# Optimization experiments

Measured on AMD Instinct MI355X. Metric: run time of the kernel, lower is better.

The kernel has to match this reference:

```python
import jax, jax.numpy as jnp
import numpy as np

N_HEADS = 16
MAX_LEN = 4096
D_MODEL = 1024
EPS = 1e-6


def setup_inputs() -> dict:
    key = jax.random.key(0)
    ks = jax.random.split(key, 12)
    B, L, D = 4, 4096, D_MODEL
    s = 1.0 / np.sqrt(D)
    inp = {
        "q": jax.random.normal(ks[0], (B, L, D), jnp.float32),
        "k": jax.random.normal(ks[1], (B, L, D), jnp.float32),
        "v": jax.random.normal(ks[2], (B, L, D), jnp.float32),
        "Wq": jax.random.normal(ks[3], (D, D), jnp.float32) * s,
        "bq": jax.random.normal(ks[4], (D,), jnp.float32) * s,
        "Wk": jax.random.normal(ks[5], (D, D), jnp.float32) * s,
        "bk": jax.random.normal(ks[6], (D,), jnp.float32) * s,
        "Wv": jax.random.normal(ks[7], (D, D), jnp.float32) * s,
        "bv": jax.random.normal(ks[8], (D,), jnp.float32) * s,
        "Wo": jax.random.normal(ks[9], (D, D), jnp.float32) * s,
        "bo": jax.random.normal(ks[10], (D,), jnp.float32) * s,
    }
    return inp


def _cos_attn(q, k, v, Wq, bq, Wk, bk, Wv, bv, Wo, bo):
    B, Lq, D = q.shape
    Lk = k.shape[1]
    H = N_HEADS
    hd = D // H
    # torch Linear: x @ W^T + b
    qh = (q @ Wq.T + bq).reshape(B, Lq, H, hd).transpose(0, 2, 1, 3)  # b h l d
    kh = (k @ Wk.T + bk).reshape(B, Lk, H, hd).transpose(0, 2, 1, 3)
    vh = (v @ Wv.T + bv).reshape(B, Lk, H, hd).transpose(0, 2, 1, 3)
    qh = jax.nn.relu(qh)
    kh = jax.nn.relu(kh)
    # weight_index buffer: pi*(1..max_len)/(2*max_len), shape (1,1,L,1)
    idx = (np.pi * jnp.arange(1, MAX_LEN + 1, dtype=jnp.float32) / (2 * MAX_LEN))
    qi = idx[:Lq][None, None, :, None]
    ki = idx[:Lk][None, None, :, None]
    q_ = jnp.concatenate([qh * jnp.sin(qi), qh * jnp.cos(qi)], axis=-1)  # b h l 2d
    k_ = jnp.concatenate([kh * jnp.sin(ki), kh * jnp.cos(ki)], axis=-1)
    kv_ = jnp.einsum("bnld,bnlm->bndm", k_, vh)  # b h 2d d
    z_ = 1.0 / jnp.maximum(jnp.einsum("bnld,bnd->bnl", q_, jnp.sum(k_, axis=2)), EPS)
    attn = jnp.einsum("bnld,bndm,bnl->bnlm", q_, kv_, z_)  # b h l d
    attn = attn.transpose(0, 2, 1, 3).reshape(B, Lq, D)
    return attn @ Wo.T + bo  # dropout: eval mode (identity)


def reference(q, k, v, Wq, bq, Wk, bk, Wv, bv, Wo, bo):
    return _cos_attn(q, k, v, Wq, bq, Wk, bk, Wv, bv, Wo, bo)
```

## Files before the change

kernel.cpp:

```cpp
#include <hip/hip_runtime.h>

typedef __bf16 bf16x8 __attribute__((ext_vector_type(8)));
typedef float f32x4 __attribute__((ext_vector_type(4)));

#define PI_F 3.14159265358979323846f

__device__ __forceinline__ unsigned short f2bf(float f) {
  unsigned u = __builtin_bit_cast(unsigned, f);
  u += 0x7fffu + ((u >> 16) & 1u);
  return (unsigned short)(u >> 16);
}

__device__ __forceinline__ unsigned scale_pair(unsigned w, float f) {
  const float lo = __builtin_bit_cast(float, w << 16);
  const float hi = __builtin_bit_cast(float, w & 0xffff0000u);
  return (unsigned)f2bf(lo * f) | ((unsigned)f2bf(hi * f) << 16);
}

#define GLD16(gp, lp)                                          \
  __builtin_amdgcn_global_load_lds(                            \
      (const __attribute__((address_space(1))) void*)(gp),     \
      (__attribute__((address_space(3))) void*)(lp), 16, 0, 0)

struct AReg { float4 a0, a1, a2, a3, a4, a5, a6, a7; };

__device__ __forceinline__ uint4 cvtpk16(float4 x, float4 y) {
  unsigned c0, c1, c2, c3;
  asm("v_cvt_pk_bf16_f32 %0, %1, %2" : "=v"(c0) : "v"(x.x), "v"(x.y));
  asm("v_cvt_pk_bf16_f32 %0, %1, %2" : "=v"(c1) : "v"(x.z), "v"(x.w));
  asm("v_cvt_pk_bf16_f32 %0, %1, %2" : "=v"(c2) : "v"(y.x), "v"(y.y));
  asm("v_cvt_pk_bf16_f32 %0, %1, %2" : "=v"(c3) : "v"(y.z), "v"(y.w));
  uint4 u; u.x = c0; u.y = c1; u.z = c2; u.w = c3;
  return u;
}

__device__ __forceinline__ uint2 cvtpk8(float a, float b, float c, float d) {
  unsigned lo, hi;
  asm("v_cvt_pk_bf16_f32 %0, %1, %2" : "=v"(lo) : "v"(a), "v"(b));
  asm("v_cvt_pk_bf16_f32 %0, %1, %2" : "=v"(hi) : "v"(c), "v"(d));
  uint2 r; r.x = lo; r.y = hi;
  return r;
}

__device__ __forceinline__ void unpack8(uint4 w, float* f) {
  f[0] = __builtin_bit_cast(float, w.x << 16);
  f[1] = __builtin_bit_cast(float, w.x & 0xffff0000u);
  f[2] = __builtin_bit_cast(float, w.y << 16);
  f[3] = __builtin_bit_cast(float, w.y & 0xffff0000u);
  f[4] = __builtin_bit_cast(float, w.z << 16);
  f[5] = __builtin_bit_cast(float, w.z & 0xffff0000u);
  f[6] = __builtin_bit_cast(float, w.w << 16);
  f[7] = __builtin_bit_cast(float, w.w & 0xffff0000u);
}

__global__ __launch_bounds__(256) void convert_w(
    const float* __restrict__ Wq, const float* __restrict__ Wk,
    const float* __restrict__ Wv, const float* __restrict__ Wo,
    unsigned short* __restrict__ Wqb, unsigned short* __restrict__ Wkb,
    unsigned short* __restrict__ Wvb, unsigned short* __restrict__ Wob) {
  const int region = blockIdx.y;
  const float* s; unsigned short* d;
  switch (region) {
    case 0: s = Wq; d = Wqb; break;
    case 1: s = Wk; d = Wkb; break;
    case 2: s = Wv; d = Wvb; break;
    default: s = Wo; d = Wob; break;
  }
  const float4* s4 = (const float4*)s;
  ushort4* d4 = (ushort4*)d;
  const int n4 = 262144;
  for (int i = blockIdx.x * 256 + threadIdx.x; i < n4; i += gridDim.x * 256) {
    float4 f = s4[i];
    ushort4 o;
    o.x = f2bf(f.x); o.y = f2bf(f.y); o.z = f2bf(f.z); o.w = f2bf(f.w);
    d4[i] = o;
  }
}

template <int MODE, bool AF32>
__global__ __launch_bounds__(512, 2) void gemm256(
    const void* __restrict__ Ain, const unsigned short* __restrict__ Bw,
    const float* __restrict__ bias, void* __restrict__ out) {
  constexpr int K = 1024, NKT = 16;
  __shared__ unsigned short S[65536];
  const int tid = threadIdx.x;
  const int wave = tid >> 6, lane = tid & 63;
  const int fr = lane & 15, fq = lane >> 4;
  const int wr = wave >> 2, wc = wave & 3;
  const int cpx = gridDim.x >> 3;
  const int wg = (blockIdx.x & 7) * cpx + (blockIdx.x >> 3);
  const int mt = wg >> 2, ntile = wg & 3;
  const int m0 = mt * 256, n0 = ntile * 256;

  const int srow = tid >> 3;
  const int ac16 = tid & 7;
  const int scolE = ((ac16 << 4) ^ ((srow & 7) << 4)) >> 1;
  const unsigned short* bSrc = Bw + (size_t)(n0 + srow) * K + scolE;
  const unsigned short* aSrcB =
      AF32 ? (const unsigned short*)nullptr
           : ((const unsigned short*)Ain + (size_t)(m0 + srow) * K + scolE);
  const float* A32 = (const float*)Ain;
  const int awoff = (ac16 ^ (srow & 7)) << 3;
  AReg R;

#define BSTAGE(kt_, buf_) do {                                                     \
    const int kc_ = (kt_) * 64;                                                    \
    GLD16(bSrc + kc_,                  S + (buf_) * 32768 + 16384 + wave * 512);   \
    GLD16(bSrc + (size_t)65536 + kc_,  S + (buf_) * 32768 + 20480 + wave * 512);   \
    GLD16(bSrc + (size_t)131072 + kc_, S + (buf_) * 32768 + 24576 + wave * 512);   \
    GLD16(bSrc + (size_t)196608 + kc_, S + (buf_) * 32768 + 28672 + wave * 512);   \
  } while (0)

#define ASTAGE(kt_, buf_) do {                                                     \
    const int kc_ = (kt_) * 64;                                                    \
    GLD16(aSrcB + kc_,                  S + (buf_) * 32768 +     0 + wave * 512);  \
    GLD16(aSrcB + (size_t)65536 + kc_,  S + (buf_) * 32768 +  4096 + wave * 512);  \
    GLD16(aSrcB + (size_t)131072 + kc_, S + (buf_) * 32768 +  8192 + wave * 512);  \
    GLD16(aSrcB + (size_t)196608 + kc_, S + (buf_) * 32768 + 12288 + wave * 512);  \
  } while (0)

#define ALOAD_ALL(kt_) do {                                                        \
    const int kc_ = (kt_) * 64;                                                    \
    const float4* p_;                                                              \
    p_ = (const float4*)(A32 + (size_t)(m0 + srow) * K + kc_) + ac16 * 2;          \
    R.a0 = p_[0]; R.a1 = p_[1];                                                    \
    p_ = (const float4*)(A32 + (size_t)(m0 + 64 + srow) * K + kc_) + ac16 * 2;     \
    R.a2 = p_[0]; R.a3 = p_[1];                                                    \
    p_ = (const float4*)(A32 + (size_t)(m0 + 128 + srow) * K + kc_) + ac16 * 2;    \
    R.a4 = p_[0]; R.a5 = p_[1];                                                    \
    p_ = (const float4*)(A32 + (size_t)(m0 + 192 + srow) * K + kc_) + ac16 * 2;    \
    R.a6 = p_[0]; R.a7 = p_[1];                                                    \
  } while (0)

#define AWRITE_ALL(buf_) do {                                                      \
    unsigned short* dst_ = &S[(buf_) * 32768 + srow * 64 + awoff];                 \
    *(uint4*)(dst_)         = cvtpk16(R.a0, R.a1);                                 \
    *(uint4*)(dst_ + 4096)  = cvtpk16(R.a2, R.a3);                                 \
    *(uint4*)(dst_ + 8192)  = cvtpk16(R.a4, R.a5);                                 \
    *(uint4*)(dst_ + 12288) = cvtpk16(R.a6, R.a7);                                 \
  } while (0)

  const int xorv = (fr & 7) << 4;
  const unsigned cbE0 = (unsigned)(((fq * 16) ^ xorv) >> 1);
  const unsigned cbE1 = (unsigned)(((64 + fq * 16) ^ xorv) >> 1);

  f32x4 acc[8][4] = {};
  if constexpr (AF32) {
    ALOAD_ALL(0);
    BSTAGE(0, 0);
    AWRITE_ALL(0);
  } else {
    BSTAGE(0, 0);
    ASTAGE(0, 0);
  }
  asm volatile("s_waitcnt vmcnt(0) lgkmcnt(0)" ::: "memory");
  __syncthreads();

  for (int kt = 0; kt < NKT; ++kt) {
    const int buf = kt & 1;
    const unsigned aB = (unsigned)(buf * 32768 + wr * 8192 + fr * 64);
    const unsigned bB = (unsigned)(buf * 32768 + 16384 + (wc >> 1) * 8192 +
                                   ((wc & 1) * 64 + fr) * 64);
    bf16x8 af[4][2], b0[2][2], b1[2][2];
#pragma unroll
    for (int mm = 0; mm < 4; ++mm) {
      const unsigned r = aB + (unsigned)(mm * 1024);
      af[mm][0] = *(const bf16x8*)&S[r + cbE0];
      af[mm][1] = *(const bf16x8*)&S[r + cbE1];
    }
#pragma unroll
    for (int nn = 0; nn < 2; ++nn) {
      const unsigned r0 = bB + (unsigned)(nn * 1024);
      b0[nn][0] = *(const bf16x8*)&S[r0 + cbE0];
      b0[nn][1] = *(const bf16x8*)&S[r0 + cbE1];
      const unsigned r1 = bB + (unsigned)((2 + nn) * 1024);
      b1[nn][0] = *(const bf16x8*)&S[r1 + cbE0];
      b1[nn][1] = *(const bf16x8*)&S[r1 + cbE1];
    }
    if (kt + 1 < NKT) {
      if constexpr (AF32) {
        ALOAD_ALL(kt + 1);
        BSTAGE(kt + 1, buf ^ 1);
      } else {
        BSTAGE(kt + 1, buf ^ 1);
        ASTAGE(kt + 1, buf ^ 1);
      }
    }
    __builtin_amdgcn_s_barrier();
    __builtin_amdgcn_s_setprio(1);
#pragma unroll
    for (int mm = 0; mm < 4; ++mm) {
#pragma unroll
      for (int nn = 0; nn < 2; ++nn) {
        acc[mm][nn] = __builtin_amdgcn_mfma_f32_16x16x32_bf16(af[mm][0], b0[nn][0], acc[mm][nn], 0, 0, 0);
        acc[mm][nn] = __builtin_amdgcn_mfma_f32_16x16x32_bf16(af[mm][1], b0[nn][1], acc[mm][nn], 0, 0, 0);
        acc[mm][2 + nn] = __builtin_amdgcn_mfma_f32_16x16x32_bf16(af[mm][0], b1[nn][0], acc[mm][2 + nn], 0, 0, 0);
        acc[mm][2 + nn] = __builtin_amdgcn_mfma_f32_16x16x32_bf16(af[mm][1], b1[nn][1], acc[mm][2 + nn], 0, 0, 0);
      }
    }
    __builtin_amdgcn_s_setprio(0);
    __builtin_amdgcn_s_barrier();
#pragma unroll
    for (int mm = 0; mm < 4; ++mm) {
      const unsigned r = aB + (unsigned)((4 + mm) * 1024);
      af[mm][0] = *(const bf16x8*)&S[r + cbE0];
      af[mm][1] = *(const bf16x8*)&S[r + cbE1];
    }
    if constexpr (AF32) {
      if (kt + 1 < NKT) AWRITE_ALL(buf ^ 1);
    }
    __builtin_amdgcn_s_barrier();
    __builtin_amdgcn_s_setprio(1);
#pragma unroll
    for (int mm = 0; mm < 4; ++mm) {
#pragma unroll
      for (int nn = 0; nn < 2; ++nn) {
        acc[4 + mm][nn] = __builtin_amdgcn_mfma_f32_16x16x32_bf16(af[mm][0], b0[nn][0], acc[4 + mm][nn], 0, 0, 0);
        acc[4 + mm][nn] = __builtin_amdgcn_mfma_f32_16x16x32_bf16(af[mm][1], b0[nn][1], acc[4 + mm][nn], 0, 0, 0);
        acc[4 + mm][2 + nn] = __builtin_amdgcn_mfma_f32_16x16x32_bf16(af[mm][0], b1[nn][0], acc[4 + mm][2 + nn], 0, 0, 0);
        acc[4 + mm][2 + nn] = __builtin_amdgcn_mfma_f32_16x16x32_bf16(af[mm][1], b1[nn][1], acc[4 + mm][2 + nn], 0, 0, 0);
      }
    }
    __builtin_amdgcn_s_setprio(0);
    asm volatile("s_waitcnt vmcnt(0) lgkmcnt(0)" ::: "memory");
    __builtin_amdgcn_s_barrier();
  }
#undef BSTAGE
#undef ASTAGE
#undef ALOAD_ALL
#undef AWRITE_ALL

  const int rowb = m0 + wr * 128 + fq * 4;
  const int colb = n0 + wc * 64 + fr;
  const int rtb0 = wr * 128 + fq * 4;
  const int mlo = m0 & 4095;
  const int b16 = (m0 >> 12) << 4;
  const int hbase = n0 >> 6;

  if constexpr (MODE == 0) {
#pragma unroll
    for (int nq = 0; nq < 4; ++nq) {
      const int col = colb + nq * 16;
      const float bb = bias[col];
      const int h = col >> 6, dd = col & 63;
#pragma unroll
      for (int mq = 0; mq < 8; ++mq) {
#pragma unroll
        for (int rr = 0; rr < 4; ++rr) {
          const int i = rowb + mq * 16 + rr;
          const int b = i >> 12, l = i & 4095;
          const float val = fmaxf(acc[mq][nq][rr] + bb, 0.0f);
          ((unsigned short*)out)[((size_t)((b << 4) + h) * 4096 + l) * 64 + dd] = f2bf(val);
        }
      }
    }
  } else if constexpr (MODE == 2) {
    float* Sf = (float*)S;
    float* O = (float*)out;
    float bb4[4];
#pragma unroll
    for (int nq = 0; nq < 4; ++nq) bb4[nq] = bias[colb + nq * 16];
    const int colL = wc * 64;
#pragma unroll
    for (int h4 = 0; h4 < 4; ++h4) {
      __syncthreads();
      if (wr == (h4 >> 1)) {
        const int mqb = (h4 & 1) * 4;
#pragma unroll
        for (int mq2 = 0; mq2 < 4; ++mq2) {
          const int rl = mq2 * 16 + fq * 4;
#pragma unroll
          for (int nq = 0; nq < 4; ++nq) {
#pragma unroll
            for (int rr = 0; rr < 4; ++rr)
              Sf[(rl + rr) * 260 + colL + nq * 16 + fr] = acc[mqb + mq2][nq][rr] + bb4[nq];
          }
        }
      }
      __syncthreads();
#pragma unroll
      for (int i = 0; i < 8; ++i) {
        const int rl = wave * 8 + i;
        const int gr = m0 + h4 * 64 + rl;
        f32x4 v4 = *(const f32x4*)&Sf[rl * 260 + lane * 4];
        *(f32x4*)(O + (size_t)gr * 1024 + n0 + lane * 4) = v4;
      }
    }
  } else {
    float bb4[4];
#pragma unroll
    for (int nq = 0; nq < 4; ++nq) bb4[nq] = bias[colb + nq * 16];
#pragma unroll
    for (int mq = 0; mq < 8; ++mq)
#pragma unroll
      for (int nq = 0; nq < 4; ++nq)
#pragma unroll
        for (int rr = 0; rr < 4; ++rr) {
          float val = acc[mq][nq][rr] + bb4[nq];
          if constexpr (MODE == 5) val = fmaxf(val, 0.0f);
          acc[mq][nq][rr] = val;
        }
    unsigned short* G = (unsigned short*)out;
    __syncthreads();
#pragma unroll
    for (int mq = 0; mq < 8; ++mq) {
      const int rtb = rtb0 + mq * 16;
#pragma unroll
      for (int nq = 0; nq < 4; ++nq) {
        const int ct = wc * 64 + nq * 16 + fr;
        uint2 w = cvtpk8(acc[mq][nq][0], acc[mq][nq][1], acc[mq][nq][2], acc[mq][nq][3]);
        *(uint2*)&S[ct * 256 + (rtb ^ ((ct & 7) << 2))] = w;
      }
    }
    __syncthreads();
#pragma unroll
    for (int it = 0; it < 16; ++it) {
      const int ct = it * 16 + (tid >> 5);
      const int lo = (tid & 31) << 3;
      const int sw = (ct & 7) << 2;
      uint2 r0 = *(const uint2*)&S[ct * 256 + (lo ^ sw)];
      uint2 r1 = *(const uint2*)&S[ct * 256 + ((lo + 4) ^ sw)];
      uint4 w; w.x = r0.x; w.y = r0.y; w.z = r1.x; w.w = r1.y;
      const int h = hbase + (ct >> 6), dd = ct & 63;
      const size_t addr = ((size_t)(b16 + h) * 64 + dd) * 4096 + mlo + lo;
      *(uint4*)(G + addr) = w;
    }
  }
}

__global__ __launch_bounds__(256, 2) void kv_gemm(
    const unsigned short* __restrict__ Vt,
    const unsigned short* __restrict__ Kt,
    float* __restrict__ kvp) {
  __shared__ unsigned short As[64 * 64];
  __shared__ unsigned short Bs[128 * 64];
  __shared__ float sn[512], cn[512];
  const int tid = threadIdx.x, wave = tid >> 6, lane = tid & 63;
  const int fr = lane & 15, fq = lane >> 4;
  const int ls = blockIdx.x, bh = blockIdx.y;
  const size_t base = (size_t)bh * 64 * 4096;
  {
    float s0, c0, s1, c1;
    __sincosf(PI_F * (float)(ls * 512 + tid + 1) * (1.0f / 8192.0f), &s0, &c0);
    __sincosf(PI_F * (float)(ls * 512 + tid + 257) * (1.0f / 8192.0f), &s1, &c1);
    sn[tid] = s0; cn[tid] = c0;
    sn[tid + 256] = s1; cn[tid + 256] = c1;
  }
  f32x4 acc[5][2] = {};
  bf16x8 ones;
#pragma unroll
  for (int j = 0; j < 8; ++j) ones[j] = (__bf16)1.0f;
  for (int t = 0; t < 8; ++t) {
    const int l0 = ls * 512 + t * 64;
    __syncthreads();
#pragma unroll
    for (int j = 0; j < 2; ++j) {
      const int p = j * 256 + tid;
      const int row = p >> 3, cc = (p & 7) ^ (row & 7);
      GLD16(Vt + base + (size_t)row * 4096 + l0 + cc * 8,
            As + ((j << 8) + (wave << 6)) * 8);
    }
#pragma unroll
    for (int j = 0; j < 2; ++j) {
      const int p = j * 256 + tid;
      const int kr = p >> 3, cc = p & 7;
      const uint4 w = *(const uint4*)(Kt + base + (size_t)kr * 4096 + l0 + cc * 8);
      const int tl = t * 64 + cc * 8;
      float kf[8];
      unpack8(w, kf);
      const float4 sA = *(const float4*)&sn[tl], sB = *(const float4*)&sn[tl + 4];
      const float4 cA = *(const float4*)&cn[tl], cB = *(const float4*)&cn[tl + 4];
      float4 x0, x1;
      x0.x = kf[0] * sA.x; x0.y = kf[1] * sA.y; x0.z = kf[2] * sA.z; x0.w = kf[3] * sA.w;
      x1.x = kf[4] * sB.x; x1.y = kf[5] * sB.y; x1.z = kf[6] * sB.z; x1.w = kf[7] * sB.w;
      const uint4 wsn = cvtpk16(x0, x1);
      x0.x = kf[0] * cA.x; x0.y = kf[1] * cA.y; x0.z = kf[2] * cA.z; x0.w = kf[3] * cA.w;
      x1.x = kf[4] * cB.x; x1.y = kf[5] * cB.y; x1.z = kf[6] * cB.z; x1.w = kf[7] * cB.w;
      const uint4 wcn = cvtpk16(x0, x1);
      const int sw_ = cc ^ (kr & 7);
      *(uint4*)&Bs[(kr * 8 + sw_) * 8] = wsn;
      *(uint4*)&Bs[((kr + 64) * 8 + sw_) * 8] = wcn;
    }
    __syncthreads();
#pragma unroll
    for (int kk = 0; kk < 2; ++kk) {
      const int ch = kk * 4 + fq;
      bf16x8 a[4], b[2];
#pragma unroll
      for (int m = 0; m < 4; ++m) {
        const int r = m * 16 + fr;
        a[m] = *(const bf16x8*)&As[(r * 8 + (ch ^ (r & 7))) * 8];
      }
#pragma unroll
      for (int n = 0; n < 2; ++n) {
        const int r = wave * 32 + n * 16 + fr;
        b[n] = *(const bf16x8*)&Bs[(r * 8 + (ch ^ (r & 7))) * 8];
      }
#pragma unroll
      for (int m = 0; m < 4; ++m)
#pragma unroll
        for (int n = 0; n < 2; ++n)
          acc[m][n] = __builtin_amdgcn_mfma_f32_16x16x32_bf16(a[m], b[n], acc[m][n], 0, 0, 0);
#pragma unroll
      for (int n = 0; n < 2; ++n)
        acc[4][n] = __builtin_amdgcn_mfma_f32_16x16x32_bf16(ones, b[n], acc[4][n], 0, 0, 0);
    }
  }
  float* outp = kvp + ((size_t)bh * 8 + ls) * (65 * 128);
  const int colb = wave * 32 + fr;
#pragma unroll
  for (int n = 0; n < 2; ++n) {
    const int col = colb + n * 16;
#pragma unroll
    for (int m = 0; m < 4; ++m)
#pragma unroll
      for (int r = 0; r < 4; ++r)
        outp[(m * 16 + fq * 4 + r) * 128 + col] = acc[m][n][r];
    if (fq == 0) outp[64 * 128 + col] = acc[4][n][0];
  }
}

__global__ __launch_bounds__(256) void kv_reduce(
    const float* __restrict__ kvp, unsigned short* __restrict__ kv_ext) {
  const int bh = blockIdx.x;
  for (int e = threadIdx.x; e < 80 * 128; e += 256) {
    const int row = e >> 7, c = e & 127;
    float v = 0.0f;
    if (row < 65) {
#pragma unroll
      for (int ls = 0; ls < 8; ++ls)
        v += kvp[((size_t)bh * 8 + ls) * (65 * 128) + row * 128 + c];
    }
    kv_ext[(size_t)bh * (80 * 128) + e] = f2bf(v);
  }
}

__global__ __launch_bounds__(256) void attn_phase2(
    const unsigned short* __restrict__ Qh, const unsigned short* __restrict__ kve,
    unsigned short* __restrict__ attn) {
  __shared__ unsigned short Qs[128 * 128];
  __shared__ unsigned short Ws[80 * 128];
  const int tid = threadIdx.x, wave = tid >> 6, lane = tid & 63;
  const int fr = lane & 15, fq = lane >> 4;
  const int l0 = blockIdx.x * 128;
  const int bh = blockIdx.y, b = bh >> 4, h = bh & 15;
#pragma unroll
  for (int j = 0; j < 5; ++j) {
    const int p = j * 256 + tid;
    const int r = p >> 4, scn = p & 15;
    const int cc = scn ^ (r & 7);
    GLD16(kve + ((size_t)bh * 80 + r) * 128 + cc * 8,
          Ws + ((size_t)(j * 256 + wave * 64)) * 8);
  }
#pragma unroll
  for (int it = 0; it < 4; ++it) {
    const int qc = it * 256 + tid;
    const int r = qc >> 3, dc = qc & 7;
    const uint4 w = *(const uint4*)(Qh + ((size_t)bh * 4096 + l0 + r) * 64 + dc * 8);
    float sv, cv;
    __sincosf(PI_F * (float)(l0 + r + 1) * (1.0f / 8192.0f), &sv, &cv);
    uint4 osn, ocs;
    osn.x = scale_pair(w.x, sv); osn.y = scale_pair(w.y, sv);
    osn.z = scale_pair(w.z, sv); osn.w = scale_pair(w.w, sv);
    ocs.x = scale_pair(w.x, cv); ocs.y = scale_pair(w.y, cv);
    ocs.z = scale_pair(w.z, cv); ocs.w = scale_pair(w.w, cv);
    const int ps = r * 16 + (dc ^ (r & 7));
    *(uint4*)&Qs[ps * 8] = osn;
    *(uint4*)&Qs[(ps + 8) * 8] = ocs;
  }
  __syncthreads();
  f32x4 acc[2][5] = {};
#pragma unroll
  for (int kk = 0; kk < 4; ++kk) {
    const int cc = kk * 4 + fq;
    bf16x8 a[2], bb[5];
#pragma unroll
    for (int m = 0; m < 2; ++m) {
      const int r = wave * 32 + m * 16 + fr;
      a[m] = *(const bf16x8*)&Qs[(r * 16 + (cc ^ (r & 7))) * 8];
    }
#pragma unroll
    for (int n = 0; n < 5; ++n) {
      const int r = n * 16 + fr;
      bb[n] = *(const bf16x8*)&Ws[(r * 16 + (cc ^ (r & 7))) * 8];
    }
#pragma unroll
    for (int m = 0; m < 2; ++m)
#pragma unroll
      for (int n = 0; n < 5; ++n)
        acc[m][n] = __builtin_amdgcn_mfma_f32_16x16x32_bf16(a[m], bb[n], acc[m][n], 0, 0, 0);
  }
#pragma unroll
  for (int m = 0; m < 2; ++m) {
#pragma unroll
    for (int r = 0; r < 4; ++r) {
      const float den = __shfl(acc[m][4][r], lane & 48);
      const float z = 1.0f / fmaxf(den, 1e-6f);
      const int l = l0 + wave * 32 + m * 16 + fq * 4 + r;
      const size_t ro = ((size_t)b * 4096 + l) * 1024 + (size_t)h * 64;
#pragma unroll
      for (int n = 0; n < 4; ++n)
        attn[ro + n * 16 + fr] = f2bf(acc[m][n][r] * z);
    }
  }
}

extern "C" void kernel_launch(void* const* d_in, const int* in_sizes, int n_in,
                              void* d_out, int out_size, void* d_ws, size_t ws_size,
                              hipStream_t stream) {
  (void)in_sizes; (void)n_in; (void)out_size; (void)ws_size;
  const float* q  = (const float*)d_in[0];
  const float* k  = (const float*)d_in[1];
  const float* v  = (const float*)d_in[2];
  const float* Wq = (const float*)d_in[3];
  const float* bq = (const float*)d_in[4];
  const float* Wk = (const float*)d_in[5];
  const float* bk = (const float*)d_in[6];
  const float* Wv = (const float*)d_in[7];
  const float* bvp = (const float*)d_in[8];
  const float* Wo = (const float*)d_in[9];
  const float* bo = (const float*)d_in[10];

  char* ws = (char*)d_ws;
  unsigned short* Wqb = (unsigned short*)(ws + 0);
  unsigned short* Wkb = (unsigned short*)(ws + 2097152);
  unsigned short* Wvb = (unsigned short*)(ws + 4194304);
  unsigned short* Wob = (unsigned short*)(ws + 6291456);
  unsigned short* Qh  = (unsigned short*)(ws + 8388608);
  unsigned short* Vt  = (unsigned short*)(ws + 41943040);
  unsigned short* Kt  = (unsigned short*)(ws + 75497472);
  unsigned short* attnb = Kt;
  float* kvp          = (float*)(ws + 109051904);
  unsigned short* kve = (unsigned short*)(ws + 126091264);

  convert_w<<<dim3(128, 4), 256, 0, stream>>>(Wq, Wk, Wv, Wo, Wqb, Wkb, Wvb, Wob);
  gemm256<0, true><<<256, 512, 0, stream>>>(q, Wqb, bq, Qh);
  gemm256<5, true><<<256, 512, 0, stream>>>(k, Wkb, bk, Kt);
  gemm256<4, true><<<256, 512, 0, stream>>>(v, Wvb, bvp, Vt);
  kv_gemm<<<dim3(8, 64), 256, 0, stream>>>(Vt, Kt, kvp);
  kv_reduce<<<64, 256, 0, stream>>>(kvp, kve);
  attn_phase2<<<dim3(32, 64), 256, 0, stream>>>(Qh, kve, attnb);
  gemm256<2, false><<<256, 512, 0, stream>>>(attnb, Wob, bo, (float*)d_out);
}
```

Measured before the change: 262.5 us.

## Merge Q/K/V projection GEMMs into one launch; emit output GEMM in bf16 then expand

New measurement: 274.2 us. 1.04x slower.

```diff
diff --git a/kernel.cpp b/kernel.cpp
--- a/kernel.cpp
+++ b/kernel.cpp
@@ -77,18 +77,26 @@
   }
 }
 
-template <int MODE, bool AF32>
-__global__ __launch_bounds__(512, 2) void gemm256(
-    const void* __restrict__ Ain, const unsigned short* __restrict__ Bw,
-    const float* __restrict__ bias, void* __restrict__ out) {
+__global__ __launch_bounds__(512, 2) void gemm_qkv(
+    const float* __restrict__ q, const float* __restrict__ k, const float* __restrict__ v,
+    const unsigned short* __restrict__ Wqb, const unsigned short* __restrict__ Wkb,
+    const unsigned short* __restrict__ Wvb,
+    const float* __restrict__ bq, const float* __restrict__ bk, const float* __restrict__ bv,
+    unsigned short* __restrict__ Qh, unsigned short* __restrict__ Kt,
+    unsigned short* __restrict__ Vt) {
   constexpr int K = 1024, NKT = 16;
   __shared__ unsigned short S[65536];
+  const int seg = blockIdx.x >> 8;
+  const int bid2 = blockIdx.x & 255;
+  const float* A32 = seg == 0 ? q : (seg == 1 ? k : v);
+  const unsigned short* Bw = seg == 0 ? Wqb : (seg == 1 ? Wkb : Wvb);
+  const float* bias = seg == 0 ? bq : (seg == 1 ? bk : bv);
+
   const int tid = threadIdx.x;
   const int wave = tid >> 6, lane = tid & 63;
   const int fr = lane & 15, fq = lane >> 4;
   const int wr = wave >> 2, wc = wave & 3;
-  const int cpx = gridDim.x >> 3;
-  const int wg = (blockIdx.x & 7) * cpx + (blockIdx.x >> 3);
+  const int wg = (bid2 & 7) * 32 + (bid2 >> 3);
   const int mt = wg >> 2, ntile = wg & 3;
   const int m0 = mt * 256, n0 = ntile * 256;
 
@@ -96,10 +104,6 @@
   const int ac16 = tid & 7;
   const int scolE = ((ac16 << 4) ^ ((srow & 7) << 4)) >> 1;
   const unsigned short* bSrc = Bw + (size_t)(n0 + srow) * K + scolE;
-  const unsigned short* aSrcB =
-      AF32 ? (const unsigned short*)nullptr
-           : ((const unsigned short*)Ain + (size_t)(m0 + srow) * K + scolE);
-  const float* A32 = (const float*)Ain;
   const int awoff = (ac16 ^ (srow & 7)) << 3;
   AReg R;
 
@@ -109,14 +113,6 @@
     GLD16(bSrc + (size_t)65536 + kc_,  S + (buf_) * 32768 + 20480 + wave * 512);   \
     GLD16(bSrc + (size_t)131072 + kc_, S + (buf_) * 32768 + 24576 + wave * 512);   \
     GLD16(bSrc + (size_t)196608 + kc_, S + (buf_) * 32768 + 28672 + wave * 512);   \
-  } while (0)
-
-#define ASTAGE(kt_, buf_) do {                                                     \
-    const int kc_ = (kt_) * 64;                                                    \
-    GLD16(aSrcB + kc_,                  S + (buf_) * 32768 +     0 + wave * 512);  \
-    GLD16(aSrcB + (size_t)65536 + kc_,  S + (buf_) * 32768 +  4096 + wave * 512);  \
-    GLD16(aSrcB + (size_t)131072 + kc_, S + (buf_) * 32768 +  8192 + wave * 512);  \
-    GLD16(aSrcB + (size_t)196608 + kc_, S + (buf_) * 32768 + 12288 + wave * 512);  \
   } while (0)
 
 #define ALOAD_ALL(kt_) do {                                                        \
@@ -145,14 +141,9 @@
   const unsigned cbE1 = (unsigned)(((64 + fq * 16) ^ xorv) >> 1);
 
   f32x4 acc[8][4] = {};
-  if constexpr (AF32) {
-    ALOAD_ALL(0);
-    BSTAGE(0, 0);
-    AWRITE_ALL(0);
-  } else {
-    BSTAGE(0, 0);
-    ASTAGE(0, 0);
-  }
+  ALOAD_ALL(0);
+  BSTAGE(0, 0);
+  AWRITE_ALL(0);
   asm volatile("s_waitcnt vmcnt(0) lgkmcnt(0)" ::: "memory");
   __syncthreads();
 
@@ -178,13 +169,8 @@
       b1[nn][1] = *(const bf16x8*)&S[r1 + cbE1];
     }
     if (kt + 1 < NKT) {
-      if constexpr (AF32) {
-        ALOAD_ALL(kt + 1);
-        BSTAGE(kt + 1, buf ^ 1);
-      } else {
-        BSTAGE(kt + 1, buf ^ 1);
-        ASTAGE(kt + 1, buf ^ 1);
-      }
+      ALOAD_ALL(kt + 1);
+      BSTAGE(kt + 1, buf ^ 1);
     }
     __builtin_amdgcn_s_barrier();
     __builtin_amdgcn_s_setprio(1);
@@ -206,9 +192,7 @@
       af[mm][0] = *(const bf16x8*)&S[r + cbE0];
       af[mm][1] = *(const bf16x8*)&S[r + cbE1];
     }
-    if constexpr (AF32) {
-      if (kt + 1 < NKT) AWRITE_ALL(buf ^ 1);
-    }
+    if (kt + 1 < NKT) AWRITE_ALL(buf ^ 1);
     __builtin_amdgcn_s_barrier();
     __builtin_amdgcn_s_setprio(1);
 #pragma unroll
@@ -226,7 +210,6 @@
     __builtin_amdgcn_s_barrier();
   }
 #undef BSTAGE
-#undef ASTAGE
 #undef ALOAD_ALL
 #undef AWRITE_ALL
 
@@ -237,7 +220,7 @@
   const int b16 = (m0 >> 12) << 4;
   const int hbase = n0 >> 6;
 
-  if constexpr (MODE == 0) {
+  if (seg == 0) {
 #pragma unroll
     for (int nq = 0; nq < 4; ++nq) {
       const int col = colb + nq * 16;
@@ -250,43 +233,13 @@
           const int i = rowb + mq * 16 + rr;
           const int b = i >> 12, l = i & 4095;
           const float val = fmaxf(acc[mq][nq][rr] + bb, 0.0f);
-          ((unsigned short*)out)[((size_t)((b << 4) + h) * 4096 + l) * 64 + dd] = f2bf(val);
+          Qh[((size_t)((b << 4) + h) * 4096 + l) * 64 + dd] = f2bf(val);
         }
       }
     }
-  } else if constexpr (MODE == 2) {
-    float* Sf = (float*)S;
-    float* O = (float*)out;
-    float bb4[4];
-#pragma unroll
-    for (int nq = 0; nq < 4; ++nq) bb4[nq] = bias[colb + nq * 16];
-    const int colL = wc * 64;
-#pragma unroll
-    for (int h4 = 0; h4 < 4; ++h4) {
-      __syncthreads();
-      if (wr == (h4 >> 1)) {
-        const int mqb = (h4 & 1) * 4;
-#pragma unroll
-        for (int mq2 = 0; mq2 < 4; ++mq2) {
-          const int rl = mq2 * 16 + fq * 4;
-#pragma unroll
-          for (int nq = 0; nq < 4; ++nq) {
-#pragma unroll
-            for (int rr = 0; rr < 4; ++rr)
-              Sf[(rl + rr) * 260 + colL + nq * 16 + fr] = acc[mqb + mq2][nq][rr] + bb4[nq];
-          }
-        }
-      }
-      __syncthreads();
-#pragma unroll
-      for (int i = 0; i < 8; ++i) {
-        const int rl = wave * 8 + i;
-        const int gr = m0 + h4 * 64 + rl;
-        f32x4 v4 = *(const f32x4*)&Sf[rl * 260 + lane * 4];
-        *(f32x4*)(O + (size_t)gr * 1024 + n0 + lane * 4) = v4;
-      }
-    }
   } else {
+    const bool relu = (seg == 1);
+    unsigned short* G = (seg == 1) ? Kt : Vt;
     float bb4[4];
 #pragma unroll
     for (int nq = 0; nq < 4; ++nq) bb4[nq] = bias[colb + nq * 16];
@@ -297,10 +250,9 @@
 #pragma unroll
         for (int rr = 0; rr < 4; ++rr) {
           float val = acc[mq][nq][rr] + bb4[nq];
-          if constexpr (MODE == 5) val = fmaxf(val, 0.0f);
+          if (relu) val = fmaxf(val, 0.0f);
           acc[mq][nq][rr] = val;
         }
-    unsigned short* G = (unsigned short*)out;
     __syncthreads();
 #pragma unroll
     for (int mq = 0; mq < 8; ++mq) {
@@ -325,6 +277,164 @@
       const size_t addr = ((size_t)(b16 + h) * 64 + dd) * 4096 + mlo + lo;
       *(uint4*)(G + addr) = w;
     }
+  }
+}
+
+__global__ __launch_bounds__(512, 2) void gemm_o(
+    const unsigned short* __restrict__ Ain, const unsigned short* __restrict__ Bw,
+    const float* __restrict__ bias, unsigned short* __restrict__ out) {
+  constexpr int K = 1024, NKT = 16;
+  __shared__ unsigned short S[65536];
+  const int tid = threadIdx.x;
+  const int wave = tid >> 6, lane = tid & 63;
+  const int fr = lane & 15, fq = lane >> 4;
+  const int wr = wave >> 2, wc = wave & 3;
+  const int wg = (blockIdx.x & 7) * 32 + (blockIdx.x >> 3);
+  const int mt = wg >> 2, ntile = wg & 3;
+  const int m0 = mt * 256, n0 = ntile * 256;
+
+  const int srow = tid >> 3;
+  const int ac16 = tid & 7;
+  const int scolE = ((ac16 << 4) ^ ((srow & 7) << 4)) >> 1;
+  const unsigned short* bSrc = Bw + (size_t)(n0 + srow) * K + scolE;
+  const unsigned short* aSrcB = Ain + (size_t)(m0 + srow) * K + scolE;
+
+#define BSTAGE(kt_, buf_) do {                                                     \
+    const int kc_ = (kt_) * 64;                                                    \
+    GLD16(bSrc + kc_,                  S + (buf_) * 32768 + 16384 + wave * 512);   \
+    GLD16(bSrc + (size_t)65536 + kc_,  S + (buf_) * 32768 + 20480 + wave * 512);   \
+    GLD16(bSrc + (size_t)131072 + kc_, S + (buf_) * 32768 + 24576 + wave * 512);   \
+    GLD16(bSrc + (size_t)196608 + kc_, S + (buf_) * 32768 + 28672 + wave * 512);   \
+  } while (0)
+
+#define ASTAGE(kt_, buf_) do {                                                     \
+    const int kc_ = (kt_) * 64;                                                    \
+    GLD16(aSrcB + kc_,                  S + (buf_) * 32768 +     0 + wave * 512);  \
+    GLD16(aSrcB + (size_t)65536 + kc_,  S + (buf_) * 32768 +  4096 + wave * 512);  \
+    GLD16(aSrcB + (size_t)131072 + kc_, S + (buf_) * 32768 +  8192 + wave * 512);  \
+    GLD16(aSrcB + (size_t)196608 + kc_, S + (buf_) * 32768 + 12288 + wave * 512);  \
+  } while (0)
+
+  const int xorv = (fr & 7) << 4;
+  const unsigned cbE0 = (unsigned)(((fq * 16) ^ xorv) >> 1);
+  const unsigned cbE1 = (unsigned)(((64 + fq * 16) ^ xorv) >> 1);
+
+  f32x4 acc[8][4] = {};
+  BSTAGE(0, 0);
+  ASTAGE(0, 0);
+  asm volatile("s_waitcnt vmcnt(0)" ::: "memory");
+  __syncthreads();
+
+  for (int kt = 0; kt < NKT; ++kt) {
+    const int buf = kt & 1;
+    const unsigned aB = (unsigned)(buf * 32768 + wr * 8192 + fr * 64);
+    const unsigned bB = (unsigned)(buf * 32768 + 16384 + (wc >> 1) * 8192 +
+                                   ((wc & 1) * 64 + fr) * 64);
+    bf16x8 af[4][2], b0[2][2], b1[2][2];
+#pragma unroll
+    for (int mm = 0; mm < 4; ++mm) {
+      const unsigned r = aB + (unsigned)(mm * 1024);
+      af[mm][0] = *(const bf16x8*)&S[r + cbE0];
+      af[mm][1] = *(const bf16x8*)&S[r + cbE1];
+    }
+#pragma unroll
+    for (int nn = 0; nn < 2; ++nn) {
+      const unsigned r0 = bB + (unsigned)(nn * 1024);
+      b0[nn][0] = *(const bf16x8*)&S[r0 + cbE0];
+      b0[nn][1] = *(const bf16x8*)&S[r0 + cbE1];
+      const unsigned r1 = bB + (unsigned)((2 + nn) * 1024);
+      b1[nn][0] = *(const bf16x8*)&S[r1 + cbE0];
+      b1[nn][1] = *(const bf16x8*)&S[r1 + cbE1];
+    }
+    if (kt + 1 < NKT) {
+      BSTAGE(kt + 1, buf ^ 1);
+      ASTAGE(kt + 1, buf ^ 1);
+    }
+    __builtin_amdgcn_s_barrier();
+    __builtin_amdgcn_s_setprio(1);
+#pragma unroll
+    for (int mm = 0; mm < 4; ++mm) {
+#pragma unroll
+      for (int nn = 0; nn < 2; ++nn) {
+        acc[mm][nn] = __builtin_amdgcn_mfma_f32_16x16x32_bf16(af[mm][0], b0[nn][0], acc[mm][nn], 0, 0, 0);
+        acc[mm][nn] = __builtin_amdgcn_mfma_f32_16x16x32_bf16(af[mm][1], b0[nn][1], acc[mm][nn], 0, 0, 0);
+        acc[mm][2 + nn] = __builtin_amdgcn_mfma_f32_16x16x32_bf16(af[mm][0], b1[nn][0], acc[mm][2 + nn], 0, 0, 0);
+        acc[mm][2 + nn] = __builtin_amdgcn_mfma_f32_16x16x32_bf16(af[mm][1], b1[nn][1], acc[mm][2 + nn], 0, 0, 0);
+      }
+    }
+    __builtin_amdgcn_s_setprio(0);
+    __builtin_amdgcn_s_barrier();
+#pragma unroll
+    for (int mm = 0; mm < 4; ++mm) {
+      const unsigned r = aB + (unsigned)((4 + mm) * 1024);
+      af[mm][0] = *(const bf16x8*)&S[r + cbE0];
+      af[mm][1] = *(const bf16x8*)&S[r + cbE1];
+    }
+    __builtin_amdgcn_s_barrier();
+    __builtin_amdgcn_s_setprio(1);
+#pragma unroll
+    for (int mm = 0; mm < 4; ++mm) {
+#pragma unroll
+      for (int nn = 0; nn < 2; ++nn) {
+        acc[4 + mm][nn] = __builtin_amdgcn_mfma_f32_16x16x32_bf16(af[mm][0], b0[nn][0], acc[4 + mm][nn], 0, 0, 0);
+        acc[4 + mm][nn] = __builtin_amdgcn_mfma_f32_16x16x32_bf16(af[mm][1], b0[nn][1], acc[4 + mm][nn], 0, 0, 0);
+        acc[4 + mm][2 + nn] = __builtin_amdgcn_mfma_f32_16x16x32_bf16(af[mm][0], b1[nn][0], acc[4 + mm][2 + nn], 0, 0, 0);
+        acc[4 + mm][2 + nn] = __builtin_amdgcn_mfma_f32_16x16x32_bf16(af[mm][1], b1[nn][1], acc[4 + mm][2 + nn], 0, 0, 0);
+      }
+    }
+    __builtin_amdgcn_s_setprio(0);
+    asm volatile("s_waitcnt vmcnt(0) lgkmcnt(0)" ::: "memory");
+    __builtin_amdgcn_s_barrier();
+  }
+#undef BSTAGE
+#undef ASTAGE
+
+  const int colb = n0 + wc * 64 + fr;
+  float* Sf = (float*)S;
+  float bb4[4];
+#pragma unroll
+  for (int nq = 0; nq < 4; ++nq) bb4[nq] = bias[colb + nq * 16];
+  const int colL = wc * 64;
+#pragma unroll
+  for (int h4 = 0; h4 < 4; ++h4) {
+    __syncthreads();
+    if (wr == (h4 >> 1)) {
+      const int mqb = (h4 & 1) * 4;
+#pragma unroll
+      for (int mq2 = 0; mq2 < 4; ++mq2) {
+        const int rl = mq2 * 16 + fq * 4;
+#pragma unroll
+        for (int nq = 0; nq < 4; ++nq) {
+#pragma unroll
+          for (int rr = 0; rr < 4; ++rr)
+            Sf[(rl + rr) * 260 + colL + nq * 16 + fr] = acc[mqb + mq2][nq][rr] + bb4[nq];
+        }
+      }
+    }
+    __syncthreads();
+#pragma unroll
+    for (int i = 0; i < 8; ++i) {
+      const int rl = wave * 8 + i;
+      const int gr = m0 + h4 * 64 + rl;
+      f32x4 v4 = *(const f32x4*)&Sf[rl * 260 + lane * 4];
+      uint2 w = cvtpk8(v4.x, v4.y, v4.z, v4.w);
+      *(uint2*)(out + (size_t)gr * 1024 + n0 + lane * 4) = w;
+    }
+  }
+}
+
+__global__ __launch_bounds__(256) void expand_bf16_f32(
+    const unsigned short* __restrict__ in, float* __restrict__ out) {
+  const int stride = gridDim.x * 256;
+  for (int i = blockIdx.x * 256 + threadIdx.x; i < 2097152; i += stride) {
+    uint4 w = ((const uint4*)in)[i];
+    float f[8];
+    unpack8(w, f);
+    f32x4 lo, hi;
+    lo.x = f[0]; lo.y = f[1]; lo.z = f[2]; lo.w = f[3];
+    hi.x = f[4]; hi.y = f[5]; hi.z = f[6]; hi.w = f[7];
+    ((f32x4*)out)[i * 2] = lo;
+    ((f32x4*)out)[i * 2 + 1] = hi;
   }
 }
 
@@ -530,15 +640,15 @@
   unsigned short* Vt  = (unsigned short*)(ws + 41943040);
   unsigned short* Kt  = (unsigned short*)(ws + 75497472);
   unsigned short* attnb = Kt;
+  unsigned short* obf = Qh;
   float* kvp          = (float*)(ws + 109051904);
   unsigned short* kve = (unsigned short*)(ws + 126091264);
 
   convert_w<<<dim3(128, 4), 256, 0, stream>>>(Wq, Wk, Wv, Wo, Wqb, Wkb, Wvb, Wob);
-  gemm256<0, true><<<256, 512, 0, stream>>>(q, Wqb, bq, Qh);
-  gemm256<5, true><<<256, 512, 0, stream>>>(k, Wkb, bk, Kt);
-  gemm256<4, true><<<256, 512, 0, stream>>>(v, Wvb, bvp, Vt);
+  gemm_qkv<<<768, 512, 0, stream>>>(q, k, v, Wqb, Wkb, Wvb, bq, bk, bvp, Qh, Kt, Vt);
   kv_gemm<<<dim3(8, 64), 256, 0, stream>>>(Vt, Kt, kvp);
   kv_reduce<<<64, 256, 0, stream>>>(kvp, kve);
   attn_phase2<<<dim3(32, 64), 256, 0, stream>>>(Qh, kve, attnb);
-  gemm256<2, false><<<256, 512, 0, stream>>>(attnb, Wob, bo, (float*)d_out);
-}
+  gemm_o<<<256, 512, 0, stream>>>(attnb, Wob, bo, obf);
+  expand_bf16_f32<<<2048, 256, 0, stream>>>(obf, (float*)d_out);
+}
```
